# Kernel tuning notes

Hardware: AMD Instinct MI355X
Metric: run time of the kernel (lower is better)

Reference implementation:

```python
import jax, jax.numpy as jnp
from jax import lax
import numpy as np


def setup_inputs() -> dict:
    key = jax.random.key(0)
    ks = jax.random.split(key, 10)
    B, T, D, U = 2048, 200, 64, 64
    return {
        "x": jax.random.normal(ks[0], (B, T, D), dtype=jnp.float32),
        "att_scores": jax.random.uniform(ks[1], (B, T, 1), dtype=jnp.float32),
        "h0": jnp.zeros((B, U), dtype=jnp.float32),
        "w_ir": jax.random.normal(ks[2], (D, U), dtype=jnp.float32),
        "w_hr": jax.random.normal(ks[3], (U, U), dtype=jnp.float32),
        "b_ir": jax.random.normal(ks[4], (U,), dtype=jnp.float32),
        "b_hr": jax.random.normal(ks[5], (U,), dtype=jnp.float32),
        "w_ih": jax.random.normal(ks[6], (D, U), dtype=jnp.float32),
        "w_hh": jax.random.normal(ks[7], (U, U), dtype=jnp.float32),
        "b_ih": jax.random.normal(ks[8], (U,), dtype=jnp.float32),
        "b_hh": jax.random.normal(ks[9], (U,), dtype=jnp.float32),
    }


def reference(x, att_scores, h0, w_ir, w_hr, b_ir, b_hr, w_ih, w_hh, b_ih, b_hh):
    # Precompute input projections for all timesteps (one big GEMM each).
    pre_r = jnp.einsum('btd,du->btu', x, w_ir) + b_ir + b_hr  # [B,T,U]
    pre_h = jnp.einsum('btd,du->btu', x, w_ih) + b_ih          # [B,T,U]

    def step(h, inp):
        pr, ph, at = inp                                # [B,U],[B,U],[B,1]
        r = jax.nn.sigmoid(pr + h @ w_hr)               # reset gate
        h_cand = jnp.tanh(ph + r * (h @ w_hh + b_hh))   # candidate state
        h_new = (1.0 - at) * h + at * h_cand            # attention-gated update
        return h_new, h_new

    xs = (pre_r.transpose(1, 0, 2),
          pre_h.transpose(1, 0, 2),
          att_scores.transpose(1, 0, 2))                # time-major
    _, hs = lax.scan(step, h0, xs)                      # hs: [T,B,U]
    return hs.transpose(1, 0, 2)                        # [B,T,U]
```

## Files before the change

### kernel.cpp

```cpp
#include <hip/hip_runtime.h>


typedef float f32x2 __attribute__((ext_vector_type(2)));

constexpr int BATCH = 2048;
constexpr int T_STEPS = 200;
constexpr int UDIM = 64;
constexpr int NROWS = BATCH * T_STEPS;

#define STR_(x) #x
#define STR(x) STR_(x)

#define PTRLO(p) ((unsigned)(unsigned long long)(const void*)(p))
#define PTRHI(p) ((unsigned)(((unsigned long long)(const void*)(p)) >> 32))

__device__ __forceinline__ float lane_bcast(float v, int lane) {
    return __builtin_bit_cast(float, __builtin_amdgcn_readlane(__builtin_bit_cast(int, v), lane));
}
__device__ __forceinline__ float fast_sigmoid(float z) {
    return __builtin_amdgcn_rcpf(1.0f + __expf(-z));
}
__device__ __forceinline__ float fast_tanh(float z) {
    return 1.0f - 2.0f * __builtin_amdgcn_rcpf(__expf(2.0f * z) + 1.0f);
}

#define WLD(R,O) "global_load_dword v" STR(R) ", v[10:11], off offset:" STR(O) "\n\t"
#define WBUMP \
  "v_add_co_u32 v10, vcc, 0x1000, v10\n\t" \
  "v_addc_co_u32 v11, vcc, 0, v11, vcc\n\t"

#define WIN16(R0,R1,R2,R3,R4,R5,R6,R7,R8,R9,R10,R11,R12,R13,R14,R15) \
  WLD(R0,0) WLD(R1,256) WLD(R2,512) WLD(R3,768) \
  WLD(R4,1024) WLD(R5,1280) WLD(R6,1536) WLD(R7,1792) \
  WLD(R8,2048) WLD(R9,2304) WLD(R10,2560) WLD(R11,2816) \
  WLD(R12,3072) WLD(R13,3328) WLD(R14,3584) WLD(R15,3840)

#define WLOAD_A \
  WIN16(64,65,66,67,68,69,70,71,72,73,74,75,76,77,78,79) WBUMP \
  WIN16(80,81,82,83,84,85,86,87,88,89,90,91,92,93,94,95) WBUMP \
  WIN16(96,97,98,99,100,101,102,103,104,105,106,107,108,109,110,111) WBUMP \
  WIN16(112,113,114,115,116,117,118,119,120,121,122,123,124,125,126,127)

#define WLOAD_B \
  WIN16(128,129,130,131,132,133,134,135,136,137,138,139,140,141,142,143) WBUMP \
  WIN16(144,145,146,147,148,149,150,151,152,153,154,155,156,157,158,159) WBUMP \
  WIN16(160,161,162,163,164,165,166,167,168,169,170,171,172,173,174,175) WBUMP \
  WIN16(176,177,178,179,180,181,182,183,184,185,186,187,188,189,190,191)

#define LDSREADS \
  "ds_read_b128 v[192:195], v29\n\t" \
  "ds_read_b128 v[196:199], v29 offset:16\n\t" \
  "ds_read_b128 v[200:203], v29 offset:32\n\t" \
  "ds_read_b128 v[204:207], v29 offset:48\n\t" \
  "ds_read_b128 v[208:211], v29 offset:64\n\t" \
  "ds_read_b128 v[212:215], v29 offset:80\n\t" \
  "ds_read_b128 v[216:219], v29 offset:96\n\t" \
  "ds_read_b128 v[220:223], v29 offset:112\n\t" \
  "ds_read_b128 v[224:227], v29 offset:128\n\t" \
  "ds_read_b128 v[228:231], v29 offset:144\n\t" \
  "ds_read_b128 v[232:235], v29 offset:160\n\t" \
  "ds_read_b128 v[236:239], v29 offset:176\n\t" \
  "ds_read_b128 v[240:243], v29 offset:192\n\t" \
  "ds_read_b128 v[244:247], v29 offset:208\n\t" \
  "ds_read_b128 v[248:251], v29 offset:224\n\t" \
  "ds_read_b128 v[252:255], v29 offset:240\n\t"

#define PKQ(W, Q0,Q1,Q2,Q3, A0,A1,A2,A3, B0,B1,B2,B3) \
  "s_waitcnt lgkmcnt(" STR(W) ")\n\t" \
  "v_pk_fma_f32 v[32:33], v[" STR(Q0) ":" STR(Q1) "], v[" STR(A0) ":" STR(A1) "], v[32:33]\n\t" \
  "v_pk_fma_f32 v[36:37], v[" STR(Q0) ":" STR(Q1) "], v[" STR(B0) ":" STR(B1) "], v[36:37]\n\t" \
  "v_pk_fma_f32 v[34:35], v[" STR(Q2) ":" STR(Q3) "], v[" STR(A2) ":" STR(A3) "], v[34:35]\n\t" \
  "v_pk_fma_f32 v[38:39], v[" STR(Q2) ":" STR(Q3) "], v[" STR(B2) ":" STR(B3) "], v[38:39]\n\t"

#define DOTCONSUME \
  PKQ(15, 192,193,194,195,  64,65,66,67,     128,129,130,131) \
  PKQ(14, 196,197,198,199,  68,69,70,71,     132,133,134,135) \
  PKQ(13, 200,201,202,203,  72,73,74,75,     136,137,138,139) \
  PKQ(12, 204,205,206,207,  76,77,78,79,     140,141,142,143) \
  PKQ(11, 208,209,210,211,  80,81,82,83,     144,145,146,147) \
  PKQ(10, 212,213,214,215,  84,85,86,87,     148,149,150,151) \
  PKQ(9,  216,217,218,219,  88,89,90,91,     152,153,154,155) \
  PKQ(8,  220,221,222,223,  92,93,94,95,     156,157,158,159) \
  PKQ(7,  224,225,226,227,  96,97,98,99,     160,161,162,163) \
  PKQ(6,  228,229,230,231,  100,101,102,103, 164,165,166,167) \
  PKQ(5,  232,233,234,235,  104,105,106,107, 168,169,170,171) \
  PKQ(4,  236,237,238,239,  108,109,110,111, 172,173,174,175) \
  PKQ(3,  240,241,242,243,  112,113,114,115, 176,177,178,179) \
  PKQ(2,  244,245,246,247,  116,117,118,119, 180,181,182,183) \
  PKQ(1,  248,249,250,251,  120,121,122,123, 184,185,186,187) \
  PKQ(0,  252,253,254,255,  124,125,126,127, 188,189,190,191)

#define ACC_ZERO \
  "v_mov_b32 v32, 0\n\t" "v_mov_b32 v33, 0\n\t" \
  "v_mov_b32 v34, 0\n\t" "v_mov_b32 v35, 0\n\t" \
  "v_mov_b32 v36, 0\n\t" "v_mov_b32 v37, 0\n\t" \
  "v_mov_b32 v38, 0\n\t" "v_mov_b32 v39, 0\n\t"

#define ACLOBBERS \
  "v8","v9","v10","v11","v12","v13","v14","v15","v16","v17", \
  "v28","v29", \
  "v32","v33","v34","v35","v36","v37","v38","v39","v40","v41","v42","v43", \
  "v44","v45","v46","v50","v51","v52","v53", \
  "v64","v65","v66","v67","v68","v69","v70","v71", \
  "v72","v73","v74","v75","v76","v77","v78","v79", \
  "v80","v81","v82","v83","v84","v85","v86","v87", \
  "v88","v89","v90","v91","v92","v93","v94","v95", \
  "v96","v97","v98","v99","v100","v101","v102","v103", \
  "v104","v105","v106","v107","v108","v109","v110","v111", \
  "v112","v113","v114","v115","v116","v117","v118","v119", \
  "v120","v121","v122","v123","v124","v125","v126","v127", \
  "v128","v129","v130","v131","v132","v133","v134","v135", \
  "v136","v137","v138","v139","v140","v141","v142","v143", \
  "v144","v145","v146","v147","v148","v149","v150","v151", \
  "v152","v153","v154","v155","v156","v157","v158","v159", \
  "v160","v161","v162","v163","v164","v165","v166","v167", \
  "v168","v169","v170","v171","v172","v173","v174","v175", \
  "v176","v177","v178","v179","v180","v181","v182","v183", \
  "v184","v185","v186","v187","v188","v189","v190","v191", \
  "v192","v193","v194","v195","v196","v197","v198","v199", \
  "v200","v201","v202","v203","v204","v205","v206","v207", \
  "v208","v209","v210","v211","v212","v213","v214","v215", \
  "v216","v217","v218","v219","v220","v221","v222","v223", \
  "v224","v225","v226","v227","v228","v229","v230","v231", \
  "v232","v233","v234","v235","v236","v237","v238","v239", \
  "v240","v241","v242","v243","v244","v245","v246","v247", \
  "v248","v249","v250","v251","v252","v253","v254","v255", \
  "s48","s49","s50","vcc","scc","memory"

__global__ __launch_bounds__(256, 2) void rec_kernel(
    const f32x2* __restrict__ pre, const float* __restrict__ att,
    const float* __restrict__ h0,  const float* __restrict__ w_hr,
    const float* __restrict__ w_hh,const float* __restrict__ b_hh,
    float* __restrict__ out)
{
    const int u   = threadIdx.x & 63;
    const int row = (int)((blockIdx.x * blockDim.x + threadIdx.x) >> 6);

    __shared__ __align__(16) float hbuf[4][UDIM];
    const unsigned lrb = (unsigned)(unsigned long long)(&hbuf[threadIdx.x >> 6][0]);
    const unsigned lwa = lrb + 4u * (unsigned)u;

    const float* wa = w_hr + u;
    const float* wb = w_hh + u;
    const f32x2* pp = pre + (size_t)row * T_STEPS * UDIM + u;
    const float* ap = att + (size_t)row * T_STEPS;
    float*       op = out + (size_t)row * T_STEPS * UDIM + u;
    const float h0v = h0[(size_t)row * UDIM + u];
    const float bgv = b_hh[u];

    asm volatile(
        "v_mov_b32 v10, %[walo]\n\t" "v_mov_b32 v11, %[wahi]\n\t"
        WLOAD_A
        "v_mov_b32 v10, %[wblo]\n\t" "v_mov_b32 v11, %[wbhi]\n\t"
        WLOAD_B
        "v_mov_b32 v12, %[prelo]\n\t" "v_mov_b32 v13, %[prehi]\n\t"
        "v_mov_b32 v14, %[attlo]\n\t" "v_mov_b32 v15, %[atthi]\n\t"
        "v_mov_b32 v16, %[outlo]\n\t" "v_mov_b32 v17, %[outhi]\n\t"
        "v_mov_b32 v8, %[h0v]\n\t"
        "v_mov_b32 v9, %[bgv]\n\t"
        "v_mov_b32 v28, %[lwa]\n\t"
        "v_mov_b32 v29, %[lrb]\n\t"
        "global_load_dwordx2 v[40:41], v[12:13], off\n\t"
        "global_load_dword v42, v[14:15], off\n\t"
        "v_add_co_u32 v12, vcc, 0x200, v12\n\t"
        "v_addc_co_u32 v13, vcc, 0, v13, vcc\n\t"
        "v_add_co_u32 v14, vcc, 4, v14\n\t"
        "v_addc_co_u32 v15, vcc, 0, v15, vcc\n\t"
        "s_waitcnt vmcnt(0)\n\t"
        "v_mov_b32 v44, v40\n\t" "v_mov_b32 v45, v41\n\t" "v_mov_b32 v46, v42\n\t"
        "global_load_dwordx2 v[40:41], v[12:13], off\n\t"
        "global_load_dword v42, v[14:15], off\n\t"
        "v_add_co_u32 v12, vcc, 0x200, v12\n\t"
        "v_addc_co_u32 v13, vcc, 0, v13, vcc\n\t"
        "v_add_co_u32 v14, vcc, 4, v14\n\t"
        "v_addc_co_u32 v15, vcc, 0, v15, vcc\n\t"
        "ds_write_b32 v28, v8\n\t"
        "s_waitcnt lgkmcnt(0)\n\t"
        LDSREADS
        "s_movk_i32 s48, 200\n\t"
        "Lrec%=:\n\t"
        ACC_ZERO
        DOTCONSUME
        "v_add_f32 v50, v32, v33\n\t"
        "v_add_f32 v51, v34, v35\n\t"
        "v_add_f32 v52, v36, v37\n\t"
        "v_add_f32 v53, v38, v39\n\t"
        "v_add_f32 v50, v50, v51\n\t"
        "v_add_f32 v52, v52, v53\n\t"
        "v_add_f32 v50, v44, v50\n\t"
        "v_add_f32 v52, v9, v52\n\t"
        "v_mul_f32 v50, 0xbfb8aa3b, v50\n\t"
        "v_exp_f32 v50, v50\n\t"
        "s_nop 1\n\t"
        "v_add_f32 v50, 1.0, v50\n\t"
        "v_rcp_f32 v50, v50\n\t"
        "s_nop 1\n\t"
        "v_mul_f32 v52, v50, v52\n\t"
        "v_add_f32 v52, v45, v52\n\t"
        "v_mul_f32 v52, 0x4038aa3b, v52\n\t"
        "v_exp_f32 v52, v52\n\t"
        "s_nop 1\n\t"
        "v_add_f32 v52, 1.0, v52\n\t"
        "v_rcp_f32 v52, v52\n\t"
        "s_nop 1\n\t"
        "v_fma_f32 v52, -2.0, v52, 1.0\n\t"
        "v_sub_f32 v53, v52, v8\n\t"
        "v_fmac_f32 v8, v46, v53\n\t"
        "ds_write_b32 v28, v8\n\t"
        "s_waitcnt vmcnt(2)\n\t"
        "v_mov_b32 v43, v8\n\t"
        "global_store_dword v[16:17], v43, off\n\t"
        "v_add_co_u32 v16, vcc, 0x100, v16\n\t"
        "v_addc_co_u32 v17, vcc, 0, v17, vcc\n\t"
        "s_waitcnt vmcnt(1)\n\t"
        "v_mov_b32 v44, v40\n\t" "v_mov_b32 v45, v41\n\t" "v_mov_b32 v46, v42\n\t"
        "global_load_dwordx2 v[40:41], v[12:13], off\n\t"
        "global_load_dword v42, v[14:15], off\n\t"
        "s_sub_u32 s48, s48, 1\n\t"
        "s_cmp_ge_u32 s48, 3\n\t"
        "s_cselect_b32 s49, 0x200, 0\n\t"
        "s_cselect_b32 s50, 4, 0\n\t"
        "v_add_co_u32 v12, vcc, s49, v12\n\t"
        "v_addc_co_u32 v13, vcc, 0, v13, vcc\n\t"
        "v_add_co_u32 v14, vcc, s50, v14\n\t"
        "v_addc_co_u32 v15, vcc, 0, v15, vcc\n\t"
        "s_waitcnt lgkmcnt(0)\n\t"
        LDSREADS
        "s_cmp_lg_u32 s48, 0\n\t"
        "s_cbranch_scc1 Lrec%=\n\t"
        "s_waitcnt vmcnt(0) lgkmcnt(0)\n\t"
        :
        : [walo]"v"(PTRLO(wa)), [wahi]"v"(PTRHI(wa)),
          [wblo]"v"(PTRLO(wb)), [wbhi]"v"(PTRHI(wb)),
          [prelo]"v"(PTRLO(pp)), [prehi]"v"(PTRHI(pp)),
          [attlo]"v"(PTRLO(ap)), [atthi]"v"(PTRHI(ap)),
          [outlo]"v"(PTRLO(op)), [outhi]"v"(PTRHI(op)),
          [h0v]"v"(h0v), [bgv]"v"(bgv),
          [lwa]"v"(lwa), [lrb]"v"(lrb)
        : ACLOBBERS);
}

__global__ __launch_bounds__(256, 3) void proj_kernel(
    const float* __restrict__ x,
    const float* __restrict__ w_ir,
    const float* __restrict__ w_ih,
    const float* __restrict__ b_ir,
    const float* __restrict__ b_hr,
    const float* __restrict__ b_ih,
    f32x2* __restrict__ pre)
{
    const int u = threadIdx.x & 63;

    f32x2 w2[UDIM];
    #pragma unroll
    for (int j = 0; j < UDIM; ++j) {
        w2[j].x = w_ir[j * UDIM + u];
        w2[j].y = w_ih[j * UDIM + u];
    }
    const float br = b_ir[u] + b_hr[u];
    const float bh = b_ih[u];

    const int nwaves = (int)((gridDim.x * blockDim.x) >> 6);
    const int wid = (int)((blockIdx.x * blockDim.x + threadIdx.x) >> 6);

    const int ngroups = NROWS / 4;
    const float* xp = x + u;

    long r = (long)wid * 4;
    float xa = xp[(r + 0) * UDIM];
    float xb = xp[(r + 1) * UDIM];
    float xc = xp[(r + 2) * UDIM];
    float xd = xp[(r + 3) * UDIM];

    for (int g = wid; g < ngroups; g += nwaves) {
        const int gn = (g + nwaves < ngroups) ? (g + nwaves) : g;
        const long rn = (long)gn * 4;
        float na = xp[(rn + 0) * UDIM];
        float nb = xp[(rn + 1) * UDIM];
        float nc = xp[(rn + 2) * UDIM];
        float nd = xp[(rn + 3) * UDIM];

        f32x2* po = pre + (long)g * 4 * UDIM + u;

        #pragma unroll
        for (int k = 0; k < 4; ++k) {
            const float xv = (k == 0) ? xa : (k == 1) ? xb : (k == 2) ? xc : xd;
            f32x2 accA; accA.x = br;  accA.y = bh;
            f32x2 accB; accB.x = 0.f; accB.y = 0.f;
            #pragma unroll
            for (int j = 0; j < UDIM; j += 2) {
                const float s0 = lane_bcast(xv, j);
                const float s1 = lane_bcast(xv, j + 1);
                accA.x = fmaf(s0, w2[j].x,     accA.x);
                accA.y = fmaf(s0, w2[j].y,     accA.y);
                accB.x = fmaf(s1, w2[j + 1].x, accB.x);
                accB.y = fmaf(s1, w2[j + 1].y, accB.y);
            }
            f32x2 o; o.x = accA.x + accB.x; o.y = accA.y + accB.y;
            po[(long)k * UDIM] = o;
        }

        xa = na; xb = nb; xc = nc; xd = nd;
    }
}

__global__ __launch_bounds__(256) void agru_fused_kernel(
    const float* __restrict__ x, const float* __restrict__ att,
    const float* __restrict__ h0,
    const float* __restrict__ w_ir, const float* __restrict__ w_hr,
    const float* __restrict__ b_ir, const float* __restrict__ b_hr,
    const float* __restrict__ w_ih, const float* __restrict__ w_hh,
    const float* __restrict__ b_ih, const float* __restrict__ b_hh,
    float* __restrict__ out)
{
    __shared__ float lds[4 * UDIM * UDIM];
    const int tid = threadIdx.x;
    #pragma unroll
    for (int i = 0; i < 16; ++i) {
        int e = tid + 256 * i;
        lds[e] = w_ir[e]; lds[4096 + e] = w_ih[e];
        lds[8192 + e] = w_hr[e]; lds[12288 + e] = w_hh[e];
    }
    __syncthreads();

    const int wave = tid >> 6;
    const int u = tid & 63;
    const int r0 = blockIdx.x * 8 + wave * 2;
    const int r1 = r0 + 1;

    float h_0 = h0[r0 * UDIM + u];
    float h_1 = h0[r1 * UDIM + u];
    const float bR = b_ir[u] + b_hr[u];
    const float bH = b_ih[u];
    const float bG = b_hh[u];

    const float* xp0 = x + (long)r0 * T_STEPS * UDIM + u;
    const float* xp1 = x + (long)r1 * T_STEPS * UDIM + u;
    const float* ap0 = att + (long)r0 * T_STEPS;
    const float* ap1 = att + (long)r1 * T_STEPS;
    float* op0 = out + (long)r0 * T_STEPS * UDIM + u;
    float* op1 = out + (long)r1 * T_STEPS * UDIM + u;

    float xv0 = xp0[0], xv1 = xp1[0], a0 = ap0[0], a1 = ap1[0];

    for (int t = 0; t < T_STEPS; ++t) {
        const int tn = (t + 1 < T_STEPS) ? (t + 1) : t;
        float nxv0 = xp0[(long)tn * UDIM], nxv1 = xp1[(long)tn * UDIM];
        float na0 = ap0[tn], na1 = ap1[tn];

        float accR0 = bR, accR1 = bR, accH0 = bH, accH1 = bH, accG0 = bG, accG1 = bG;
        #pragma unroll
        for (int j = 0; j < 64; ++j) {
            const float wir = lds[j * 64 + u];
            const float wih = lds[4096 + j * 64 + u];
            const float whr = lds[8192 + j * 64 + u];
            const float whh = lds[12288 + j * 64 + u];
            const float xj0 = lane_bcast(xv0, j);
            const float xj1 = lane_bcast(xv1, j);
            const float hj0 = lane_bcast(h_0, j);
            const float hj1 = lane_bcast(h_1, j);
            accR0 = fmaf(xj0, wir, accR0); accR0 = fmaf(hj0, whr, accR0);
            accH0 = fmaf(xj0, wih, accH0); accG0 = fmaf(hj0, whh, accG0);
            accR1 = fmaf(xj1, wir, accR1); accR1 = fmaf(hj1, whr, accR1);
            accH1 = fmaf(xj1, wih, accH1); accG1 = fmaf(hj1, whh, accG1);
        }
        const float r0g = fast_sigmoid(accR0);
        const float r1g = fast_sigmoid(accR1);
        const float hc0 = fast_tanh(fmaf(r0g, accG0, accH0));
        const float hc1 = fast_tanh(fmaf(r1g, accG1, accH1));
        h_0 = fmaf(a0, hc0 - h_0, h_0);
        h_1 = fmaf(a1, hc1 - h_1, h_1);
        op0[(long)t * UDIM] = h_0;
        op1[(long)t * UDIM] = h_1;
        xv0 = nxv0; xv1 = nxv1; a0 = na0; a1 = na1;
    }
}

extern "C" void kernel_launch(void* const* d_in, const int* in_sizes, int n_in,
                              void* d_out, int out_size, void* d_ws, size_t ws_size,
                              hipStream_t stream) {
    (void)in_sizes; (void)n_in; (void)out_size;

    const float* x    = (const float*)d_in[0];
    const float* att  = (const float*)d_in[1];
    const float* h0   = (const float*)d_in[2];
    const float* w_ir = (const float*)d_in[3];
    const float* w_hr = (const float*)d_in[4];
    const float* b_ir = (const float*)d_in[5];
    const float* b_hr = (const float*)d_in[6];
    const float* w_ih = (const float*)d_in[7];
    const float* w_hh = (const float*)d_in[8];
    const float* b_ih = (const float*)d_in[9];
    const float* b_hh = (const float*)d_in[10];
    float* out = (float*)d_out;

    const size_t pre_bytes = (size_t)NROWS * UDIM * sizeof(f32x2);

    if (ws_size >= pre_bytes) {
        f32x2* pre = (f32x2*)d_ws;
        proj_kernel<<<dim3(1024), dim3(256), 0, stream>>>(
            x, w_ir, w_ih, b_ir, b_hr, b_ih, pre);
        rec_kernel<<<dim3(512), dim3(256), 0, stream>>>(
            pre, att, h0, w_hr, w_hh, b_hh, out);
    } else {
        agru_fused_kernel<<<dim3(256), dim3(256), 0, stream>>>(
            x, att, h0, w_ir, w_hr, b_ir, b_hr, w_ih, w_hh, b_ih, b_hh, out);
    }
}
```

Measured before the change: 245.2 us.

## Process two batch rows per wave in recurrence kernel to amortize weight registers

Each wavefront now advances two independent batch rows through the recurrence at once. Both rows share the weight registers, and the two dependency chains are interleaved so exp/rcp latency and LDS reads of one row hide behind the other. Pointers move to scalar registers with SGPR-base addressing to cut VALU address arithmetic. In exchange the grid is halved to 256 blocks with launch bounds of one block per CU, so fewer waves are resident and parallelism across the GPU is lower.

```diff
diff --git a/kernel.cpp b/kernel.cpp
--- a/kernel.cpp
+++ b/kernel.cpp
@@ -14,6 +14,9 @@
 #define PTRLO(p) ((unsigned)(unsigned long long)(const void*)(p))
 #define PTRHI(p) ((unsigned)(((unsigned long long)(const void*)(p)) >> 32))
 
+__device__ __forceinline__ unsigned rfl(unsigned x) {
+    return (unsigned)__builtin_amdgcn_readfirstlane((int)x);
+}
 __device__ __forceinline__ float lane_bcast(float v, int lane) {
     return __builtin_bit_cast(float, __builtin_amdgcn_readlane(__builtin_bit_cast(int, v), lane));
 }
@@ -24,10 +27,8 @@
     return 1.0f - 2.0f * __builtin_amdgcn_rcpf(__expf(2.0f * z) + 1.0f);
 }
 
-#define WLD(R,O) "global_load_dword v" STR(R) ", v[10:11], off offset:" STR(O) "\n\t"
-#define WBUMP \
-  "v_add_co_u32 v10, vcc, 0x1000, v10\n\t" \
-  "v_addc_co_u32 v11, vcc, 0, v11, vcc\n\t"
+#define WLD(R,O) "global_load_dword v" STR(R) ", v14, s[56:57] offset:" STR(O) "\n\t"
+#define WBUMP "s_add_u32 s56, s56, 0x1000\n\ts_addc_u32 s57, s57, 0\n\t"
 
 #define WIN16(R0,R1,R2,R3,R4,R5,R6,R7,R8,R9,R10,R11,R12,R13,R14,R15) \
   WLD(R0,0) WLD(R1,256) WLD(R2,512) WLD(R3,768) \
@@ -47,23 +48,26 @@
   WIN16(160,161,162,163,164,165,166,167,168,169,170,171,172,173,174,175) WBUMP \
   WIN16(176,177,178,179,180,181,182,183,184,185,186,187,188,189,190,191)
 
-#define LDSREADS \
-  "ds_read_b128 v[192:195], v29\n\t" \
-  "ds_read_b128 v[196:199], v29 offset:16\n\t" \
-  "ds_read_b128 v[200:203], v29 offset:32\n\t" \
-  "ds_read_b128 v[204:207], v29 offset:48\n\t" \
-  "ds_read_b128 v[208:211], v29 offset:64\n\t" \
-  "ds_read_b128 v[212:215], v29 offset:80\n\t" \
-  "ds_read_b128 v[216:219], v29 offset:96\n\t" \
-  "ds_read_b128 v[220:223], v29 offset:112\n\t" \
-  "ds_read_b128 v[224:227], v29 offset:128\n\t" \
-  "ds_read_b128 v[228:231], v29 offset:144\n\t" \
-  "ds_read_b128 v[232:235], v29 offset:160\n\t" \
-  "ds_read_b128 v[236:239], v29 offset:176\n\t" \
-  "ds_read_b128 v[240:243], v29 offset:192\n\t" \
-  "ds_read_b128 v[244:247], v29 offset:208\n\t" \
-  "ds_read_b128 v[248:251], v29 offset:224\n\t" \
-  "ds_read_b128 v[252:255], v29 offset:240\n\t"
+#define READ_A_LO \
+  "ds_read_b128 v[192:195], v29\n\t"            "ds_read_b128 v[196:199], v29 offset:16\n\t" \
+  "ds_read_b128 v[200:203], v29 offset:32\n\t"  "ds_read_b128 v[204:207], v29 offset:48\n\t" \
+  "ds_read_b128 v[208:211], v29 offset:64\n\t"  "ds_read_b128 v[212:215], v29 offset:80\n\t" \
+  "ds_read_b128 v[216:219], v29 offset:96\n\t"  "ds_read_b128 v[220:223], v29 offset:112\n\t"
+#define READ_A_HI \
+  "ds_read_b128 v[192:195], v29 offset:128\n\t" "ds_read_b128 v[196:199], v29 offset:144\n\t" \
+  "ds_read_b128 v[200:203], v29 offset:160\n\t" "ds_read_b128 v[204:207], v29 offset:176\n\t" \
+  "ds_read_b128 v[208:211], v29 offset:192\n\t" "ds_read_b128 v[212:215], v29 offset:208\n\t" \
+  "ds_read_b128 v[216:219], v29 offset:224\n\t" "ds_read_b128 v[220:223], v29 offset:240\n\t"
+#define READ_B_LO \
+  "ds_read_b128 v[224:227], v31\n\t"            "ds_read_b128 v[228:231], v31 offset:16\n\t" \
+  "ds_read_b128 v[232:235], v31 offset:32\n\t"  "ds_read_b128 v[236:239], v31 offset:48\n\t" \
+  "ds_read_b128 v[240:243], v31 offset:64\n\t"  "ds_read_b128 v[244:247], v31 offset:80\n\t" \
+  "ds_read_b128 v[248:251], v31 offset:96\n\t"  "ds_read_b128 v[252:255], v31 offset:112\n\t"
+#define READ_B_HI \
+  "ds_read_b128 v[224:227], v31 offset:128\n\t" "ds_read_b128 v[228:231], v31 offset:144\n\t" \
+  "ds_read_b128 v[232:235], v31 offset:160\n\t" "ds_read_b128 v[236:239], v31 offset:176\n\t" \
+  "ds_read_b128 v[240:243], v31 offset:192\n\t" "ds_read_b128 v[244:247], v31 offset:208\n\t" \
+  "ds_read_b128 v[248:251], v31 offset:224\n\t" "ds_read_b128 v[252:255], v31 offset:240\n\t"
 
 #define PKQ(W, Q0,Q1,Q2,Q3, A0,A1,A2,A3, B0,B1,B2,B3) \
   "s_waitcnt lgkmcnt(" STR(W) ")\n\t" \
@@ -71,8 +75,14 @@
   "v_pk_fma_f32 v[36:37], v[" STR(Q0) ":" STR(Q1) "], v[" STR(B0) ":" STR(B1) "], v[36:37]\n\t" \
   "v_pk_fma_f32 v[34:35], v[" STR(Q2) ":" STR(Q3) "], v[" STR(A2) ":" STR(A3) "], v[34:35]\n\t" \
   "v_pk_fma_f32 v[38:39], v[" STR(Q2) ":" STR(Q3) "], v[" STR(B2) ":" STR(B3) "], v[38:39]\n\t"
-
-#define DOTCONSUME \
+#define PKQB(W, Q0,Q1,Q2,Q3, A0,A1,A2,A3, B0,B1,B2,B3) \
+  "s_waitcnt lgkmcnt(" STR(W) ")\n\t" \
+  "v_pk_fma_f32 v[54:55], v[" STR(Q0) ":" STR(Q1) "], v[" STR(A0) ":" STR(A1) "], v[54:55]\n\t" \
+  "v_pk_fma_f32 v[58:59], v[" STR(Q0) ":" STR(Q1) "], v[" STR(B0) ":" STR(B1) "], v[58:59]\n\t" \
+  "v_pk_fma_f32 v[56:57], v[" STR(Q2) ":" STR(Q3) "], v[" STR(A2) ":" STR(A3) "], v[56:57]\n\t" \
+  "v_pk_fma_f32 v[60:61], v[" STR(Q2) ":" STR(Q3) "], v[" STR(B2) ":" STR(B3) "], v[60:61]\n\t"
+
+#define CONSUME_A_LO \
   PKQ(15, 192,193,194,195,  64,65,66,67,     128,129,130,131) \
   PKQ(14, 196,197,198,199,  68,69,70,71,     132,133,134,135) \
   PKQ(13, 200,201,202,203,  72,73,74,75,     136,137,138,139) \
@@ -80,27 +90,47 @@
   PKQ(11, 208,209,210,211,  80,81,82,83,     144,145,146,147) \
   PKQ(10, 212,213,214,215,  84,85,86,87,     148,149,150,151) \
   PKQ(9,  216,217,218,219,  88,89,90,91,     152,153,154,155) \
-  PKQ(8,  220,221,222,223,  92,93,94,95,     156,157,158,159) \
-  PKQ(7,  224,225,226,227,  96,97,98,99,     160,161,162,163) \
-  PKQ(6,  228,229,230,231,  100,101,102,103, 164,165,166,167) \
-  PKQ(5,  232,233,234,235,  104,105,106,107, 168,169,170,171) \
-  PKQ(4,  236,237,238,239,  108,109,110,111, 172,173,174,175) \
-  PKQ(3,  240,241,242,243,  112,113,114,115, 176,177,178,179) \
-  PKQ(2,  244,245,246,247,  116,117,118,119, 180,181,182,183) \
-  PKQ(1,  248,249,250,251,  120,121,122,123, 184,185,186,187) \
-  PKQ(0,  252,253,254,255,  124,125,126,127, 188,189,190,191)
-
-#define ACC_ZERO \
-  "v_mov_b32 v32, 0\n\t" "v_mov_b32 v33, 0\n\t" \
-  "v_mov_b32 v34, 0\n\t" "v_mov_b32 v35, 0\n\t" \
-  "v_mov_b32 v36, 0\n\t" "v_mov_b32 v37, 0\n\t" \
-  "v_mov_b32 v38, 0\n\t" "v_mov_b32 v39, 0\n\t"
-
-#define ACLOBBERS \
-  "v8","v9","v10","v11","v12","v13","v14","v15","v16","v17", \
-  "v28","v29", \
-  "v32","v33","v34","v35","v36","v37","v38","v39","v40","v41","v42","v43", \
-  "v44","v45","v46","v50","v51","v52","v53", \
+  PKQ(8,  220,221,222,223,  92,93,94,95,     156,157,158,159)
+#define CONSUME_B_LO \
+  PKQB(15, 224,225,226,227,  64,65,66,67,     128,129,130,131) \
+  PKQB(14, 228,229,230,231,  68,69,70,71,     132,133,134,135) \
+  PKQB(13, 232,233,234,235,  72,73,74,75,     136,137,138,139) \
+  PKQB(12, 236,237,238,239,  76,77,78,79,     140,141,142,143) \
+  PKQB(11, 240,241,242,243,  80,81,82,83,     144,145,146,147) \
+  PKQB(10, 244,245,246,247,  84,85,86,87,     148,149,150,151) \
+  PKQB(9,  248,249,250,251,  88,89,90,91,     152,153,154,155) \
+  PKQB(8,  252,253,254,255,  92,93,94,95,     156,157,158,159)
+#define CONSUME_A_HI \
+  PKQ(15, 192,193,194,195,  96,97,98,99,     160,161,162,163) \
+  PKQ(14, 196,197,198,199,  100,101,102,103, 164,165,166,167) \
+  PKQ(13, 200,201,202,203,  104,105,106,107, 168,169,170,171) \
+  PKQ(12, 204,205,206,207,  108,109,110,111, 172,173,174,175) \
+  PKQ(11, 208,209,210,211,  112,113,114,115, 176,177,178,179) \
+  PKQ(10, 212,213,214,215,  116,117,118,119, 180,181,182,183) \
+  PKQ(9,  216,217,218,219,  120,121,122,123, 184,185,186,187) \
+  PKQ(8,  220,221,222,223,  124,125,126,127, 188,189,190,191)
+#define CONSUME_B_HI \
+  PKQB(7,  224,225,226,227,  96,97,98,99,     160,161,162,163) \
+  PKQB(6,  228,229,230,231,  100,101,102,103, 164,165,166,167) \
+  PKQB(5,  232,233,234,235,  104,105,106,107, 168,169,170,171) \
+  PKQB(4,  236,237,238,239,  108,109,110,111, 172,173,174,175) \
+  PKQB(3,  240,241,242,243,  112,113,114,115, 176,177,178,179) \
+  PKQB(2,  244,245,246,247,  116,117,118,119, 180,181,182,183) \
+  PKQB(1,  248,249,250,251,  120,121,122,123, 184,185,186,187) \
+  PKQB(0,  252,253,254,255,  124,125,126,127, 188,189,190,191)
+
+#define ACC_ZERO_AB \
+  "v_mov_b32 v32, 0\n\t" "v_mov_b32 v33, 0\n\t" "v_mov_b32 v34, 0\n\t" "v_mov_b32 v35, 0\n\t" \
+  "v_mov_b32 v36, 0\n\t" "v_mov_b32 v37, 0\n\t" "v_mov_b32 v38, 0\n\t" "v_mov_b32 v39, 0\n\t" \
+  "v_mov_b32 v54, 0\n\t" "v_mov_b32 v55, 0\n\t" "v_mov_b32 v56, 0\n\t" "v_mov_b32 v57, 0\n\t" \
+  "v_mov_b32 v58, 0\n\t" "v_mov_b32 v59, 0\n\t" "v_mov_b32 v60, 0\n\t" "v_mov_b32 v61, 0\n\t"
+
+#define REC_CLOBBERS \
+  "v8","v9","v12","v13","v14","v15","v16", \
+  "v24","v25","v26","v27","v28","v29","v30","v31", \
+  "v32","v33","v34","v35","v36","v37","v38","v39", \
+  "v40","v41","v42","v43","v44","v45","v46","v47","v48","v49","v50", \
+  "v51","v52","v53","v54","v55","v56","v57","v58","v59","v60","v61","v62", \
   "v64","v65","v66","v67","v68","v69","v70","v71", \
   "v72","v73","v74","v75","v76","v77","v78","v79", \
   "v80","v81","v82","v83","v84","v85","v86","v87", \
@@ -125,119 +155,188 @@
   "v232","v233","v234","v235","v236","v237","v238","v239", \
   "v240","v241","v242","v243","v244","v245","v246","v247", \
   "v248","v249","v250","v251","v252","v253","v254","v255", \
-  "s48","s49","s50","vcc","scc","memory"
-
-__global__ __launch_bounds__(256, 2) void rec_kernel(
+  "s40","s41","s42","s43","s44","s45","s46","s47", \
+  "s52","s53","s54","s55","s56","s57","s60","s61","s62", \
+  "vcc","scc","memory"
+
+__global__ __launch_bounds__(256, 1) void rec_kernel(
     const f32x2* __restrict__ pre, const float* __restrict__ att,
     const float* __restrict__ h0,  const float* __restrict__ w_hr,
     const float* __restrict__ w_hh,const float* __restrict__ b_hh,
     float* __restrict__ out)
 {
     const int u   = threadIdx.x & 63;
-    const int row = (int)((blockIdx.x * blockDim.x + threadIdx.x) >> 6);
-
-    __shared__ __align__(16) float hbuf[4][UDIM];
-    const unsigned lrb = (unsigned)(unsigned long long)(&hbuf[threadIdx.x >> 6][0]);
+    const int wid = (int)((blockIdx.x * blockDim.x + threadIdx.x) >> 6);
+    const int rA  = wid * 2;
+    const int rB  = rA + 1;
+
+    __shared__ __align__(16) float hbuf[4][2][UDIM];
+    const unsigned lrb = (unsigned)(unsigned long long)(&hbuf[threadIdx.x >> 6][0][0]);
     const unsigned lwa = lrb + 4u * (unsigned)u;
 
-    const float* wa = w_hr + u;
-    const float* wb = w_hh + u;
-    const f32x2* pp = pre + (size_t)row * T_STEPS * UDIM + u;
-    const float* ap = att + (size_t)row * T_STEPS;
-    float*       op = out + (size_t)row * T_STEPS * UDIM + u;
-    const float h0v = h0[(size_t)row * UDIM + u];
+    const f32x2* pA = pre + (size_t)rA * T_STEPS * UDIM;
+    const f32x2* pB = pre + (size_t)rB * T_STEPS * UDIM;
+    const float* aA = att + (size_t)rA * T_STEPS;
+    const float* aB = att + (size_t)rB * T_STEPS;
+    float*       oA = out + (size_t)rA * T_STEPS * UDIM;
+    float*       oB = out + (size_t)rB * T_STEPS * UDIM;
+
+    const unsigned walo = rfl(PTRLO(w_hr)), wahi = rfl(PTRHI(w_hr));
+    const unsigned whlo = rfl(PTRLO(w_hh)), whhi = rfl(PTRHI(w_hh));
+    const unsigned pAlo = rfl(PTRLO(pA)), pAhi = rfl(PTRHI(pA));
+    const unsigned pBlo = rfl(PTRLO(pB)), pBhi = rfl(PTRHI(pB));
+    const unsigned aAlo = rfl(PTRLO(aA)), aAhi = rfl(PTRHI(aA));
+    const unsigned aBlo = rfl(PTRLO(aB)), aBhi = rfl(PTRHI(aB));
+    const unsigned oAlo = rfl(PTRLO(oA)), oAhi = rfl(PTRHI(oA));
+    const unsigned oBlo = rfl(PTRLO(oB)), oBhi = rfl(PTRHI(oB));
+
+    const float h0A = h0[(size_t)rA * UDIM + u];
+    const float h0B = h0[(size_t)rB * UDIM + u];
     const float bgv = b_hh[u];
 
     asm volatile(
-        "v_mov_b32 v10, %[walo]\n\t" "v_mov_b32 v11, %[wahi]\n\t"
-        WLOAD_A
-        "v_mov_b32 v10, %[wblo]\n\t" "v_mov_b32 v11, %[wbhi]\n\t"
-        WLOAD_B
-        "v_mov_b32 v12, %[prelo]\n\t" "v_mov_b32 v13, %[prehi]\n\t"
-        "v_mov_b32 v14, %[attlo]\n\t" "v_mov_b32 v15, %[atthi]\n\t"
-        "v_mov_b32 v16, %[outlo]\n\t" "v_mov_b32 v17, %[outhi]\n\t"
-        "v_mov_b32 v8, %[h0v]\n\t"
-        "v_mov_b32 v9, %[bgv]\n\t"
+        "s_mov_b32 s40, %[pAlo]\n\t" "s_mov_b32 s41, %[pAhi]\n\t"
+        "s_mov_b32 s42, %[aAlo]\n\t" "s_mov_b32 s43, %[aAhi]\n\t"
+        "s_mov_b32 s44, %[oAlo]\n\t" "s_mov_b32 s45, %[oAhi]\n\t"
+        "s_mov_b32 s46, %[pBlo]\n\t" "s_mov_b32 s47, %[pBhi]\n\t"
+        "s_mov_b32 s52, %[aBlo]\n\t" "s_mov_b32 s53, %[aBhi]\n\t"
+        "s_mov_b32 s54, %[oBlo]\n\t" "s_mov_b32 s55, %[oBhi]\n\t"
         "v_mov_b32 v28, %[lwa]\n\t"
         "v_mov_b32 v29, %[lrb]\n\t"
-        "global_load_dwordx2 v[40:41], v[12:13], off\n\t"
-        "global_load_dword v42, v[14:15], off\n\t"
-        "v_add_co_u32 v12, vcc, 0x200, v12\n\t"
-        "v_addc_co_u32 v13, vcc, 0, v13, vcc\n\t"
-        "v_add_co_u32 v14, vcc, 4, v14\n\t"
-        "v_addc_co_u32 v15, vcc, 0, v15, vcc\n\t"
+        "v_add_u32 v30, 0x100, v28\n\t"
+        "v_add_u32 v31, 0x100, v29\n\t"
+        "v_sub_u32 v14, v28, v29\n\t"
+        "v_lshlrev_b32 v12, 1, v14\n\t"
+        "v_mov_b32 v13, 0\n\t"
+        "s_mov_b32 s56, %[walo]\n\t" "s_mov_b32 s57, %[wahi]\n\t"
+        WLOAD_A
+        "s_mov_b32 s56, %[whlo]\n\t" "s_mov_b32 s57, %[whhi]\n\t"
+        WLOAD_B
+        "v_mov_b32 v8, %[h0A]\n\t"
+        "v_mov_b32 v9, %[h0B]\n\t"
+        "v_mov_b32 v27, %[bgv]\n\t"
+        "global_load_dwordx2 v[40:41], v12, s[40:41]\n\t"
+        "global_load_dword v42, v13, s[42:43]\n\t"
+        "global_load_dwordx2 v[24:25], v12, s[46:47]\n\t"
+        "global_load_dword v26, v13, s[52:53]\n\t"
+        "s_add_u32 s40, s40, 0x200\n\t" "s_addc_u32 s41, s41, 0\n\t"
+        "s_add_u32 s46, s46, 0x200\n\t" "s_addc_u32 s47, s47, 0\n\t"
+        "s_add_u32 s42, s42, 4\n\t"     "s_addc_u32 s43, s43, 0\n\t"
+        "s_add_u32 s52, s52, 4\n\t"     "s_addc_u32 s53, s53, 0\n\t"
         "s_waitcnt vmcnt(0)\n\t"
         "v_mov_b32 v44, v40\n\t" "v_mov_b32 v45, v41\n\t" "v_mov_b32 v46, v42\n\t"
-        "global_load_dwordx2 v[40:41], v[12:13], off\n\t"
-        "global_load_dword v42, v[14:15], off\n\t"
-        "v_add_co_u32 v12, vcc, 0x200, v12\n\t"
-        "v_addc_co_u32 v13, vcc, 0, v13, vcc\n\t"
-        "v_add_co_u32 v14, vcc, 4, v14\n\t"
-        "v_addc_co_u32 v15, vcc, 0, v15, vcc\n\t"
+        "v_mov_b32 v48, v24\n\t" "v_mov_b32 v49, v25\n\t" "v_mov_b32 v47, v26\n\t"
+        "global_load_dwordx2 v[40:41], v12, s[40:41]\n\t"
+        "global_load_dword v42, v13, s[42:43]\n\t"
+        "global_load_dwordx2 v[24:25], v12, s[46:47]\n\t"
+        "global_load_dword v26, v13, s[52:53]\n\t"
+        "s_add_u32 s40, s40, 0x200\n\t" "s_addc_u32 s41, s41, 0\n\t"
+        "s_add_u32 s46, s46, 0x200\n\t" "s_addc_u32 s47, s47, 0\n\t"
+        "s_add_u32 s42, s42, 4\n\t"     "s_addc_u32 s43, s43, 0\n\t"
+        "s_add_u32 s52, s52, 4\n\t"     "s_addc_u32 s53, s53, 0\n\t"
         "ds_write_b32 v28, v8\n\t"
+        "ds_write_b32 v30, v9\n\t"
         "s_waitcnt lgkmcnt(0)\n\t"
-        LDSREADS
-        "s_movk_i32 s48, 200\n\t"
+        READ_A_LO
+        READ_B_LO
+        "s_movk_i32 s60, 200\n\t"
         "Lrec%=:\n\t"
-        ACC_ZERO
-        DOTCONSUME
-        "v_add_f32 v50, v32, v33\n\t"
-        "v_add_f32 v51, v34, v35\n\t"
+        ACC_ZERO_AB
+        CONSUME_A_LO
+        READ_A_HI
+        CONSUME_B_LO
+        READ_B_HI
+        CONSUME_A_HI
+        CONSUME_B_HI
+        "v_add_f32 v51, v32, v33\n\t"
+        "v_add_f32 v53, v54, v55\n\t"
+        "v_add_f32 v52, v34, v35\n\t"
+        "v_add_f32 v62, v56, v57\n\t"
+        "v_add_f32 v51, v51, v52\n\t"
+        "v_add_f32 v53, v53, v62\n\t"
         "v_add_f32 v52, v36, v37\n\t"
-        "v_add_f32 v53, v38, v39\n\t"
-        "v_add_f32 v50, v50, v51\n\t"
-        "v_add_f32 v52, v52, v53\n\t"
-        "v_add_f32 v50, v44, v50\n\t"
-        "v_add_f32 v52, v9, v52\n\t"
-        "v_mul_f32 v50, 0xbfb8aa3b, v50\n\t"
-        "v_exp_f32 v50, v50\n\t"
-        "s_nop 1\n\t"
-        "v_add_f32 v50, 1.0, v50\n\t"
-        "v_rcp_f32 v50, v50\n\t"
-        "s_nop 1\n\t"
-        "v_mul_f32 v52, v50, v52\n\t"
+        "v_add_f32 v62, v58, v59\n\t"
+        "v_add_f32 v15, v38, v39\n\t"
+        "v_add_f32 v16, v60, v61\n\t"
+        "v_add_f32 v52, v52, v15\n\t"
+        "v_add_f32 v62, v62, v16\n\t"
+        "v_add_f32 v51, v44, v51\n\t"
+        "v_add_f32 v53, v48, v53\n\t"
+        "v_add_f32 v52, v27, v52\n\t"
+        "v_add_f32 v62, v27, v62\n\t"
+        "v_mul_f32 v51, 0xbfb8aa3b, v51\n\t"
+        "v_mul_f32 v53, 0xbfb8aa3b, v53\n\t"
+        "v_exp_f32 v51, v51\n\t"
+        "v_exp_f32 v53, v53\n\t"
+        "s_nop 0\n\t"
+        "v_add_f32 v51, 1.0, v51\n\t"
+        "v_add_f32 v53, 1.0, v53\n\t"
+        "v_rcp_f32 v51, v51\n\t"
+        "v_rcp_f32 v53, v53\n\t"
+        "s_nop 0\n\t"
+        "v_mul_f32 v52, v51, v52\n\t"
+        "v_mul_f32 v62, v53, v62\n\t"
         "v_add_f32 v52, v45, v52\n\t"
+        "v_add_f32 v62, v49, v62\n\t"
         "v_mul_f32 v52, 0x4038aa3b, v52\n\t"
+        "v_mul_f32 v62, 0x4038aa3b, v62\n\t"
         "v_exp_f32 v52, v52\n\t"
-        "s_nop 1\n\t"
+        "v_exp_f32 v62, v62\n\t"
+        "s_nop 0\n\t"
         "v_add_f32 v52, 1.0, v52\n\t"
+        "v_add_f32 v62, 1.0, v62\n\t"
         "v_rcp_f32 v52, v52\n\t"
-        "s_nop 1\n\t"
+        "v_rcp_f32 v62, v62\n\t"
+        "s_nop 0\n\t"
         "v_fma_f32 v52, -2.0, v52, 1.0\n\t"
-        "v_sub_f32 v53, v52, v8\n\t"
-        "v_fmac_f32 v8, v46, v53\n\t"
+        "v_fma_f32 v62, -2.0, v62, 1.0\n\t"
+        "v_sub_f32 v15, v52, v8\n\t"
+        "v_sub_f32 v16, v62, v9\n\t"
+        "v_fmac_f32 v8, v46, v15\n\t"
+        "v_fmac_f32 v9, v47, v16\n\t"
         "ds_write_b32 v28, v8\n\t"
+        "ds_write_b32 v30, v9\n\t"
+        "s_waitcnt vmcnt(5)\n\t"
+        "v_mov_b32 v43, v8\n\t"
+        "global_store_dword v14, v43, s[44:45]\n\t"
+        "s_waitcnt vmcnt(5)\n\t"
+        "v_mov_b32 v50, v9\n\t"
+        "global_store_dword v14, v50, s[54:55]\n\t"
         "s_waitcnt vmcnt(2)\n\t"
-        "v_mov_b32 v43, v8\n\t"
-        "global_store_dword v[16:17], v43, off\n\t"
-        "v_add_co_u32 v16, vcc, 0x100, v16\n\t"
-        "v_addc_co_u32 v17, vcc, 0, v17, vcc\n\t"
-        "s_waitcnt vmcnt(1)\n\t"
         "v_mov_b32 v44, v40\n\t" "v_mov_b32 v45, v41\n\t" "v_mov_b32 v46, v42\n\t"
-        "global_load_dwordx2 v[40:41], v[12:13], off\n\t"
-        "global_load_dword v42, v[14:15], off\n\t"
-        "s_sub_u32 s48, s48, 1\n\t"
-        "s_cmp_ge_u32 s48, 3\n\t"
-        "s_cselect_b32 s49, 0x200, 0\n\t"
-        "s_cselect_b32 s50, 4, 0\n\t"
-        "v_add_co_u32 v12, vcc, s49, v12\n\t"
-        "v_addc_co_u32 v13, vcc, 0, v13, vcc\n\t"
-        "v_add_co_u32 v14, vcc, s50, v14\n\t"
-        "v_addc_co_u32 v15, vcc, 0, v15, vcc\n\t"
+        "v_mov_b32 v48, v24\n\t" "v_mov_b32 v49, v25\n\t" "v_mov_b32 v47, v26\n\t"
+        "global_load_dwordx2 v[40:41], v12, s[40:41]\n\t"
+        "global_load_dword v42, v13, s[42:43]\n\t"
+        "global_load_dwordx2 v[24:25], v12, s[46:47]\n\t"
+        "global_load_dword v26, v13, s[52:53]\n\t"
+        "s_sub_u32 s60, s60, 1\n\t"
+        "s_cmp_ge_u32 s60, 3\n\t"
+        "s_cselect_b32 s61, 0x200, 0\n\t"
+        "s_cselect_b32 s62, 4, 0\n\t"
+        "s_add_u32 s40, s40, s61\n\t" "s_addc_u32 s41, s41, 0\n\t"
+        "s_add_u32 s46, s46, s61\n\t" "s_addc_u32 s47, s47, 0\n\t"
+        "s_add_u32 s42, s42, s62\n\t" "s_addc_u32 s43, s43, 0\n\t"
+        "s_add_u32 s52, s52, s62\n\t" "s_addc_u32 s53, s53, 0\n\t"
+        "s_add_u32 s44, s44, 0x100\n\t" "s_addc_u32 s45, s45, 0\n\t"
+        "s_add_u32 s54, s54, 0x100\n\t" "s_addc_u32 s55, s55, 0\n\t"
         "s_waitcnt lgkmcnt(0)\n\t"
-        LDSREADS
-        "s_cmp_lg_u32 s48, 0\n\t"
+        READ_A_LO
+        READ_B_LO
+        "s_cmp_lg_u32 s60, 0\n\t"
         "s_cbranch_scc1 Lrec%=\n\t"
         "s_waitcnt vmcnt(0) lgkmcnt(0)\n\t"
         :
-        : [walo]"v"(PTRLO(wa)), [wahi]"v"(PTRHI(wa)),
-          [wblo]"v"(PTRLO(wb)), [wbhi]"v"(PTRHI(wb)),
-          [prelo]"v"(PTRLO(pp)), [prehi]"v"(PTRHI(pp)),
-          [attlo]"v"(PTRLO(ap)), [atthi]"v"(PTRHI(ap)),
-          [outlo]"v"(PTRLO(op)), [outhi]"v"(PTRHI(op)),
-          [h0v]"v"(h0v), [bgv]"v"(bgv),
+        : [walo]"s"(walo), [wahi]"s"(wahi),
+          [whlo]"s"(whlo), [whhi]"s"(whhi),
+          [pAlo]"s"(pAlo), [pAhi]"s"(pAhi),
+          [aAlo]"s"(aAlo), [aAhi]"s"(aAhi),
+          [oAlo]"s"(oAlo), [oAhi]"s"(oAhi),
+          [pBlo]"s"(pBlo), [pBhi]"s"(pBhi),
+          [aBlo]"s"(aBlo), [aBhi]"s"(aBhi),
+          [oBlo]"s"(oBlo), [oBhi]"s"(oBhi),
+          [h0A]"v"(h0A), [h0B]"v"(h0B), [bgv]"v"(bgv),
           [lwa]"v"(lwa), [lrb]"v"(lrb)
-        : ACLOBBERS);
+        : REC_CLOBBERS);
 }
 
 __global__ __launch_bounds__(256, 3) void proj_kernel(
@@ -400,7 +499,7 @@
         f32x2* pre = (f32x2*)d_ws;
         proj_kernel<<<dim3(1024), dim3(256), 0, stream>>>(
             x, w_ir, w_ih, b_ir, b_hr, b_ih, pre);
-        rec_kernel<<<dim3(512), dim3(256), 0, stream>>>(
+        rec_kernel<<<dim3(256), dim3(256), 0, stream>>>(
             pre, att, h0, w_hr, w_hh, b_hh, out);
     } else {
         agru_fused_kernel<<<dim3(256), dim3(256), 0, stream>>>(
```

After: 252.2 us. 1.03x slower.
